# Kernel optimization log

Hardware: AMD Instinct MI355X
Metric: run time of the kernel (lower is better)

Reference implementation:

```python
import jax, jax.numpy as jnp
import numpy as np

B, N, C = 4, 2048, 768
H = 12
D = C // H  # head_dim = 64


def setup_inputs() -> dict:
    key = jax.random.key(0)
    k1, k2, k3, k4, k5 = jax.random.split(key, 5)
    s = 0.02
    return {
        "x": jax.random.normal(k1, (B, N, C), dtype=jnp.float32),
        "qkv_w": jax.random.normal(k2, (3 * C, C), dtype=jnp.float32) * s,
        "qkv_b": jax.random.normal(k3, (3 * C,), dtype=jnp.float32) * s,
        "proj_w": jax.random.normal(k4, (C, C), dtype=jnp.float32) * s,
        "proj_b": jax.random.normal(k5, (C,), dtype=jnp.float32) * s,
    }


def reference(x, qkv_w, qkv_b, proj_w, proj_b):
    b, n, c = x.shape
    # qkv projection (torch Linear: x @ W.T + b) -> [B,N,3,H,D] -> [3,B,H,N,D]
    qkv = (x @ qkv_w.T + qkv_b).reshape(b, n, 3, H, D).transpose(2, 0, 3, 1, 4)
    q, k, v = qkv[0], qkv[1], qkv[2]
    scale = D ** (-0.5)
    attn = jnp.einsum("bhqd,bhkd->bhqk", q, k) * scale
    attn = jax.nn.softmax(attn, axis=-1)
    # dropout is identity in eval mode
    out = jnp.einsum("bhqk,bhkd->bhqd", attn, v)  # [B,H,N,D]
    out = out.transpose(0, 2, 1, 3).reshape(b, n, c)
    return out @ proj_w.T + proj_b
```

## Files before the change

### kernel.cpp

```cpp
#include <hip/hip_runtime.h>
#include <hip/hip_bf16.h>
#include <stdint.h>

typedef __bf16 bf16_t;
typedef __bf16 bf16x8 __attribute__((ext_vector_type(8)));
typedef float f32x4 __attribute__((ext_vector_type(4)));
typedef unsigned int u32x4 __attribute__((ext_vector_type(4)));

#define NB 4
#define NH 12
#define ND 64
#define NN 2048
#define NC 768

__device__ __forceinline__ void async_copy16(const bf16_t* g, bf16_t* l) {
    __builtin_amdgcn_global_load_lds((__attribute__((address_space(1))) void*)(void*)g,
                                     (__attribute__((address_space(3))) void*)l, 16, 0, 0);
}

__device__ __forceinline__ unsigned pack_bf2(float a, float b) {
    union { bf16_t e[2]; unsigned u; } t;
    t.e[0] = (bf16_t)a;
    t.e[1] = (bf16_t)b;
    return t.u;
}

__global__ void cast_kernel(const float* __restrict__ src, bf16_t* __restrict__ dst, int n4) {
    int i = blockIdx.x * blockDim.x + threadIdx.x;
    if (i >= n4) return;
    float4 v = ((const float4*)src)[i];
    union { bf16_t e[4]; uint2 u; } t;
    t.e[0] = (bf16_t)v.x; t.e[1] = (bf16_t)v.y; t.e[2] = (bf16_t)v.z; t.e[3] = (bf16_t)v.w;
    ((uint2*)dst)[i] = t.u;
}

__device__ __forceinline__ int vperm(int s) {
    return (s & 32) | (((s >> 2) & 3) << 3) | (((s >> 4) & 1) << 2) | (s & 3);
}


template <bool ISV>
__launch_bounds__(256)
__global__ void qkv_gemm_kernel(const bf16_t* __restrict__ X, const bf16_t* __restrict__ W,
                                const float* __restrict__ bias,
                                bf16_t* __restrict__ Q, bf16_t* __restrict__ K, bf16_t* __restrict__ V,
                                int n0base)
{
    __shared__ __align__(16) bf16_t sA[128 * 64];
    __shared__ __align__(16) bf16_t sB[128 * 64];
    const int tid  = threadIdx.x;
    const int lane = tid & 63;
    const int w    = tid >> 6;
    const int wm   = w & 1, wn = w >> 1;
    const int m0   = blockIdx.x * 128;
    const int n0   = n0base + blockIdx.y * 128;
    const int lrow = lane & 15;
    const int quad = lane >> 4;
    const int arow = lane >> 3;
    const int gch  = (lane & 7) ^ arow;

    const int colbase = n0 + wn * 64;

    f32x4 zero = {0.f, 0.f, 0.f, 0.f};
    f32x4 acc[4][4];
#pragma unroll
    for (int i = 0; i < 4; ++i)
#pragma unroll
        for (int j = 0; j < 4; ++j) acc[i][j] = zero;

    for (int kt = 0; kt < NC; kt += 64) {
        __syncthreads();
        for (int c = w; c < 16; c += 4) {
            async_copy16(X + (size_t)(m0 + c * 8 + arow) * NC + kt + gch * 8, sA + c * 512);
            async_copy16(W + (size_t)(n0 + c * 8 + arow) * NC + kt + gch * 8, sB + c * 512);
        }
        __syncthreads();
#pragma unroll
        for (int hh = 0; hh < 2; ++hh) {
            bf16x8 xf[4], wf[4];
#pragma unroll
            for (int i = 0; i < 4; ++i) {
                int r = wm * 64 + i * 16 + lrow;
                xf[i] = *(const bf16x8*)(sA + r * 64 + (((hh * 4 + quad) ^ (r & 7)) * 8));
            }
#pragma unroll
            for (int j = 0; j < 4; ++j) {
                int r = wn * 64 + j * 16 + lrow;
                wf[j] = *(const bf16x8*)(sB + r * 64 + (((hh * 4 + quad) ^ (r & 7)) * 8));
            }
#pragma unroll
            for (int i = 0; i < 4; ++i)
#pragma unroll
                for (int j = 0; j < 4; ++j) {
                    if (ISV)
                        acc[i][j] = __builtin_amdgcn_mfma_f32_16x16x32_bf16(xf[i], wf[j], acc[i][j], 0, 0, 0);
                    else
                        acc[i][j] = __builtin_amdgcn_mfma_f32_16x16x32_bf16(wf[j], xf[i], acc[i][j], 0, 0, 0);
                }
        }
    }

    const float qscale = 0.125f * 1.44269504088896340736f;

    if (!ISV) {
        const int t3 = colbase / NC;
        const int h  = (colbase % NC) / ND;
        bf16_t* outb = t3 ? K : Q;
#pragma unroll
        for (int j = 0; j < 4; ++j) {
            const int dcol = j * 16 + quad * 4;
            const float4 bv4 = *(const float4*)(bias + colbase + dcol);
#pragma unroll
            for (int i = 0; i < 4; ++i) {
                const int tok = m0 + wm * 64 + i * 16 + lrow;
                const int bb = tok >> 11;
                const int nn = tok & 2047;
                union { bf16_t e[4]; uint2 u; } pk;
#pragma unroll
                for (int p = 0; p < 4; ++p) {
                    float val = acc[i][j][p] + (&bv4.x)[p];
                    if (t3 == 0) val *= qscale;
                    pk.e[p] = (bf16_t)val;
                }
                *(uint2*)(outb + ((size_t)(bb * NH + h) * NN + nn) * ND + dcol) = pk.u;
            }
        }
    } else {
        const int h = (colbase - 2 * NC) / ND;
#pragma unroll
        for (int j = 0; j < 4; ++j) {
            const int d  = j * 16 + lrow;
            const float bv = bias[colbase + d];
#pragma unroll
            for (int i = 0; i < 4; ++i) {
                const int tok0 = m0 + wm * 64 + i * 16 + quad * 4;
                const int bb = tok0 >> 11;
                const int nn = tok0 & 2047;
                union { bf16_t e[4]; uint2 u; } pk;
#pragma unroll
                for (int p = 0; p < 4; ++p) pk.e[p] = (bf16_t)(acc[i][j][p] + bv);
                const int pos = (nn & ~63) | vperm(nn & 63);
                *(uint2*)(V + ((size_t)(bb * NH + h) * ND + d) * NN + pos) = pk.u;
            }
        }
    }
}

__launch_bounds__(256, 4)
__global__ void attn_kernel(const bf16_t* __restrict__ Q, const bf16_t* __restrict__ K,
                            const bf16_t* __restrict__ Vt, bf16_t* __restrict__ O)
{
    __shared__ __align__(16) bf16_t sKV[4][64 * 64];
    bf16_t* sQ = sKV[0];
    const int tid  = threadIdx.x;
    const int lane = tid & 63;
    const int w    = tid >> 6;
    const int qt   = blockIdx.x;
    const int h    = blockIdx.y;
    const int b    = blockIdx.z;
    const int lrow = lane & 15;
    const int quad = lane >> 4;
    const int arow = lane >> 3;
    const int gch  = (lane & 7) ^ arow;
    const size_t head_off = (size_t)(b * NH + h) * NN * ND;
    const bf16_t* qh = Q  + head_off;
    const bf16_t* kh = K  + head_off;
    const bf16_t* vh = Vt + head_off;

#pragma unroll
    for (int c = 0; c < 4; ++c)
        async_copy16(qh + (size_t)(qt * 128 + (w * 4 + c) * 8 + arow) * ND + gch * 8,
                     sQ + (w * 4 + c) * 512);
    __syncthreads();

    bf16x8 qb[2][2];
#pragma unroll
    for (int qi = 0; qi < 2; ++qi)
#pragma unroll
        for (int hh = 0; hh < 2; ++hh) {
            int r = w * 32 + qi * 16 + lrow;
            qb[qi][hh] = *(const bf16x8*)(sQ + r * 64 + (((hh * 4 + quad) ^ (r & 7)) * 8));
        }

    int off[4][2];
#pragma unroll
    for (int blk = 0; blk < 4; ++blk) {
        int r = blk * 16 + lrow;
        off[blk][0] = r * 64 + ((quad ^ (r & 7)) * 8);
        off[blk][1] = r * 64 + (((4 + quad) ^ (r & 7)) * 8);
    }

    f32x4 zero = {0.f, 0.f, 0.f, 0.f};
    f32x4 o[2][4];
#pragma unroll
    for (int qi = 0; qi < 2; ++qi)
#pragma unroll
        for (int db = 0; db < 4; ++db) o[qi][db] = zero;
    float l_i[2] = {0.f, 0.f};

    const bf16_t* kp = kh + (size_t)(w * 16 + arow) * ND + gch * 8;
    const bf16_t* vp = vh + (size_t)(w * 16 + arow) * NN + gch * 8;

    for (int it = 0; it < NN / 128; ++it) {
        __syncthreads();
        async_copy16(kp,               sKV[0] + w * 1024);
        async_copy16(kp + 8 * ND,      sKV[0] + w * 1024 + 512);
        async_copy16(kp + 64 * ND,     sKV[1] + w * 1024);
        async_copy16(kp + 72 * ND,     sKV[1] + w * 1024 + 512);
        async_copy16(vp,               sKV[2] + w * 1024);
        async_copy16(vp + 8 * NN,      sKV[2] + w * 1024 + 512);
        async_copy16(vp + 64,          sKV[3] + w * 1024);
        async_copy16(vp + 8 * NN + 64, sKV[3] + w * 1024 + 512);
        __syncthreads();
        kp += 128 * ND;
        vp += 128;

#pragma unroll
        for (int half = 0; half < 2; ++half) {
            const bf16_t* sKh = sKV[half];
            const bf16_t* sVh = sKV[2 + half];

            f32x4 s[2][4];
#pragma unroll
            for (int blk = 0; blk < 4; ++blk) {
                bf16x8 a0 = *(const bf16x8*)(sKh + off[blk][0]);
                bf16x8 a1 = *(const bf16x8*)(sKh + off[blk][1]);
#pragma unroll
                for (int qi = 0; qi < 2; ++qi) {
                    f32x4 z = zero;
                    z = __builtin_amdgcn_mfma_f32_16x16x32_bf16(a0, qb[qi][0], z, 0, 0, 0);
                    z = __builtin_amdgcn_mfma_f32_16x16x32_bf16(a1, qb[qi][1], z, 0, 0, 0);
                    s[qi][blk] = z;
                }
            }

            bf16x8 pe[2][2];
#pragma unroll
            for (int qi = 0; qi < 2; ++qi) {
                u32x4 pu0 = {0, 0, 0, 0}, pu1 = {0, 0, 0, 0};
                float r0 = 0.f, r1 = 0.f;
#pragma unroll
                for (int blk = 0; blk < 4; ++blk) {
                    float e0 = __builtin_amdgcn_exp2f(s[qi][blk][0]);
                    float e1 = __builtin_amdgcn_exp2f(s[qi][blk][1]);
                    float e2 = __builtin_amdgcn_exp2f(s[qi][blk][2]);
                    float e3 = __builtin_amdgcn_exp2f(s[qi][blk][3]);
                    r0 += e0 + e1;
                    r1 += e2 + e3;
                    unsigned lo = pack_bf2(e0, e1), hi = pack_bf2(e2, e3);
                    if (blk == 0)      { pu0[0] = lo; pu0[1] = hi; }
                    else if (blk == 1) { pu0[2] = lo; pu0[3] = hi; }
                    else if (blk == 2) { pu1[0] = lo; pu1[1] = hi; }
                    else               { pu1[2] = lo; pu1[3] = hi; }
                }
                pe[qi][0] = __builtin_bit_cast(bf16x8, pu0);
                pe[qi][1] = __builtin_bit_cast(bf16x8, pu1);
                l_i[qi] += r0 + r1;
            }

#pragma unroll
            for (int db = 0; db < 4; ++db) {
                bf16x8 v0 = *(const bf16x8*)(sVh + off[db][0]);
                bf16x8 v1 = *(const bf16x8*)(sVh + off[db][1]);
#pragma unroll
                for (int qi = 0; qi < 2; ++qi) {
                    o[qi][db] = __builtin_amdgcn_mfma_f32_16x16x32_bf16(v0, pe[qi][0], o[qi][db], 0, 0, 0);
                    o[qi][db] = __builtin_amdgcn_mfma_f32_16x16x32_bf16(v1, pe[qi][1], o[qi][db], 0, 0, 0);
                }
            }
        }
    }

#pragma unroll
    for (int qi = 0; qi < 2; ++qi) {
        float l = l_i[qi];
        l += __shfl_xor(l, 16);
        l += __shfl_xor(l, 32);
        const float rl = 1.0f / l;
        const int n = qt * 128 + w * 32 + qi * 16 + lrow;
        const size_t rowoff = ((size_t)(b * NN + n)) * NC + h * ND;
#pragma unroll
        for (int db = 0; db < 4; ++db) {
            union { bf16_t e[4]; uint2 u; } pk;
#pragma unroll
            for (int p = 0; p < 4; ++p) pk.e[p] = (bf16_t)(o[qi][db][p] * rl);
            *(uint2*)(O + rowoff + db * 16 + quad * 4) = pk.u;
        }
    }
}

__launch_bounds__(256)
__global__ void proj_gemm_kernel(const bf16_t* __restrict__ A, const bf16_t* __restrict__ W,
                                 const float* __restrict__ bias, float* __restrict__ out)
{
    __shared__ __align__(16) bf16_t sA[128 * 64];
    __shared__ __align__(16) bf16_t sB[128 * 64];
    const int tid  = threadIdx.x;
    const int lane = tid & 63;
    const int w    = tid >> 6;
    const int wm   = w & 1, wn = w >> 1;
    const int m0   = blockIdx.x * 128;
    const int n0   = blockIdx.y * 128;
    const int lrow = lane & 15;
    const int quad = lane >> 4;
    const int arow = lane >> 3;
    const int gch  = (lane & 7) ^ arow;

    f32x4 zero = {0.f, 0.f, 0.f, 0.f};
    f32x4 acc[4][4];
#pragma unroll
    for (int i = 0; i < 4; ++i)
#pragma unroll
        for (int j = 0; j < 4; ++j) acc[i][j] = zero;

    for (int kt = 0; kt < NC; kt += 64) {
        __syncthreads();
        for (int c = w; c < 16; c += 4) {
            async_copy16(A + (size_t)(m0 + c * 8 + arow) * NC + kt + gch * 8, sA + c * 512);
            async_copy16(W + (size_t)(n0 + c * 8 + arow) * NC + kt + gch * 8, sB + c * 512);
        }
        __syncthreads();
#pragma unroll
        for (int hh = 0; hh < 2; ++hh) {
            bf16x8 xf[4], wf[4];
#pragma unroll
            for (int i = 0; i < 4; ++i) {
                int r = wm * 64 + i * 16 + lrow;
                xf[i] = *(const bf16x8*)(sA + r * 64 + (((hh * 4 + quad) ^ (r & 7)) * 8));
            }
#pragma unroll
            for (int j = 0; j < 4; ++j) {
                int r = wn * 64 + j * 16 + lrow;
                wf[j] = *(const bf16x8*)(sB + r * 64 + (((hh * 4 + quad) ^ (r & 7)) * 8));
            }
#pragma unroll
            for (int i = 0; i < 4; ++i)
#pragma unroll
                for (int j = 0; j < 4; ++j)
                    acc[i][j] = __builtin_amdgcn_mfma_f32_16x16x32_bf16(wf[j], xf[i], acc[i][j], 0, 0, 0);
        }
    }

#pragma unroll
    for (int j = 0; j < 4; ++j) {
        const int colg0 = n0 + wn * 64 + j * 16 + quad * 4;
        const float4 bv4 = *(const float4*)(bias + colg0);
#pragma unroll
        for (int i = 0; i < 4; ++i) {
            const int tok = m0 + wm * 64 + i * 16 + lrow;
            float4 val;
#pragma unroll
            for (int p = 0; p < 4; ++p) (&val.x)[p] = acc[i][j][p] + (&bv4.x)[p];
            *(float4*)(out + (size_t)tok * NC + colg0) = val;
        }
    }
}

extern "C" void kernel_launch(void* const* d_in, const int* in_sizes, int n_in,
                              void* d_out, int out_size, void* d_ws, size_t ws_size,
                              hipStream_t stream) {
    const float* x      = (const float*)d_in[0];
    const float* qkv_w  = (const float*)d_in[1];
    const float* qkv_b  = (const float*)d_in[2];
    const float* proj_w = (const float*)d_in[3];
    const float* proj_b = (const float*)d_in[4];
    float* out = (float*)d_out;

    char* ws = (char*)d_ws;
    bf16_t* xb    = (bf16_t*)ws; ws += (size_t)8192 * 768 * 2;
    bf16_t* wqkv  = (bf16_t*)ws; ws += (size_t)2304 * 768 * 2;
    bf16_t* wproj = (bf16_t*)ws; ws += (size_t)768 * 768 * 2;
    bf16_t* qb    = (bf16_t*)ws; ws += (size_t)NB * NH * NN * ND * 2;
    bf16_t* kb    = (bf16_t*)ws; ws += (size_t)NB * NH * NN * ND * 2;
    bf16_t* vb    = (bf16_t*)ws; ws += (size_t)NB * NH * NN * ND * 2;
    bf16_t* ab    = (bf16_t*)ws; ws += (size_t)8192 * 768 * 2;

    cast_kernel<<<(8192 * 768 / 4 + 255) / 256, 256, 0, stream>>>(x, xb, 8192 * 768 / 4);
    cast_kernel<<<(2304 * 768 / 4 + 255) / 256, 256, 0, stream>>>(qkv_w, wqkv, 2304 * 768 / 4);
    cast_kernel<<<(768 * 768 / 4 + 255) / 256, 256, 0, stream>>>(proj_w, wproj, 768 * 768 / 4);

    qkv_gemm_kernel<false><<<dim3(8192 / 128, 12), 256, 0, stream>>>(xb, wqkv, qkv_b, qb, kb, vb, 0);
    qkv_gemm_kernel<true><<<dim3(8192 / 128, 6), 256, 0, stream>>>(xb, wqkv, qkv_b, qb, kb, vb, 1536);
    attn_kernel<<<dim3(NN / 128, NH, NB), 256, 0, stream>>>(qb, kb, vb, ab);
    proj_gemm_kernel<<<dim3(8192 / 128, 768 / 128), 256, 0, stream>>>(ab, wproj, proj_b, out);
}
```

Before: 238.7 us.

## Double-buffer LDS tiles in GEMM and attention kernels, merge cast launches

The QKV and projection GEMMs change from single-buffered 64-wide K tiles with two barriers per step to double-buffered 32-wide K tiles. The next tile's async global-to-LDS copy is issued before the current tile's MFMAs, so each step needs only one barrier. The attention kernel also double-buffers its 64-key K/V tiles to overlap loads with compute, and adds a barrier after reading Q from the shared buffer. The three fp32-to-bf16 cast launches become one kernel, and both GEMMs get an occupancy hint of 4 blocks. The costs are more loop iterations, more barriers in attention, and possible register pressure under the new launch bounds.

```diff
diff --git a/kernel.cpp b/kernel.cpp
--- a/kernel.cpp
+++ b/kernel.cpp
@@ -25,13 +25,21 @@
     return t.u;
 }
 
-__global__ void cast_kernel(const float* __restrict__ src, bf16_t* __restrict__ dst, int n4) {
+__global__ void cast3_kernel(const float* __restrict__ s0, bf16_t* __restrict__ d0, int n0,
+                             const float* __restrict__ s1, bf16_t* __restrict__ d1, int n1,
+                             const float* __restrict__ s2, bf16_t* __restrict__ d2, int n2) {
     int i = blockIdx.x * blockDim.x + threadIdx.x;
-    if (i >= n4) return;
-    float4 v = ((const float4*)src)[i];
+    const float* s;
+    bf16_t* d;
+    int j;
+    if (i < n0)           { s = s0; d = d0; j = i; }
+    else if (i < n0 + n1) { s = s1; d = d1; j = i - n0; }
+    else if (i < n0 + n1 + n2) { s = s2; d = d2; j = i - n0 - n1; }
+    else return;
+    float4 v = ((const float4*)s)[j];
     union { bf16_t e[4]; uint2 u; } t;
     t.e[0] = (bf16_t)v.x; t.e[1] = (bf16_t)v.y; t.e[2] = (bf16_t)v.z; t.e[3] = (bf16_t)v.w;
-    ((uint2*)dst)[i] = t.u;
+    ((uint2*)d)[j] = t.u;
 }
 
 __device__ __forceinline__ int vperm(int s) {
@@ -40,14 +48,14 @@
 
 
 template <bool ISV>
-__launch_bounds__(256)
+__launch_bounds__(256, 4)
 __global__ void qkv_gemm_kernel(const bf16_t* __restrict__ X, const bf16_t* __restrict__ W,
                                 const float* __restrict__ bias,
                                 bf16_t* __restrict__ Q, bf16_t* __restrict__ K, bf16_t* __restrict__ V,
                                 int n0base)
 {
-    __shared__ __align__(16) bf16_t sA[128 * 64];
-    __shared__ __align__(16) bf16_t sB[128 * 64];
+    __shared__ __align__(16) bf16_t sA[2][128 * 32];
+    __shared__ __align__(16) bf16_t sB[2][128 * 32];
     const int tid  = threadIdx.x;
     const int lane = tid & 63;
     const int w    = tid >> 6;
@@ -56,8 +64,12 @@
     const int n0   = n0base + blockIdx.y * 128;
     const int lrow = lane & 15;
     const int quad = lane >> 4;
-    const int arow = lane >> 3;
-    const int gch  = (lane & 7) ^ arow;
+
+    const int srow = w * 16 + (lane >> 2);
+    const int gchk = ((lane & 3) ^ (srow & 3)) * 8;
+    const bf16_t* pA = X + (size_t)(m0 + srow) * NC + gchk;
+    const bf16_t* pB = W + (size_t)(n0 + srow) * NC + gchk;
+    const int ldst = w * 512 + lane * 8;
 
     const int colbase = n0 + wn * 64;
 
@@ -68,36 +80,47 @@
 #pragma unroll
         for (int j = 0; j < 4; ++j) acc[i][j] = zero;
 
-    for (int kt = 0; kt < NC; kt += 64) {
+    int offA[4], offB[4];
+#pragma unroll
+    for (int i = 0; i < 4; ++i) {
+        int rA = wm * 64 + i * 16 + lrow;
+        int rB = wn * 64 + i * 16 + lrow;
+        offA[i] = rA * 32 + ((quad ^ (rA & 3)) * 8);
+        offB[i] = rB * 32 + ((quad ^ (rB & 3)) * 8);
+    }
+
+    async_copy16(pA,           sA[0] + ldst);
+    async_copy16(pA + 64 * NC, sA[0] + ldst + 2048);
+    async_copy16(pB,           sB[0] + ldst);
+    async_copy16(pB + 64 * NC, sB[0] + ldst + 2048);
+    pA += 32; pB += 32;
+    __syncthreads();
+
+    int cur = 0;
+    for (int it = 0; it < NC / 32; ++it) {
+        if (it + 1 < NC / 32) {
+            async_copy16(pA,           sA[cur ^ 1] + ldst);
+            async_copy16(pA + 64 * NC, sA[cur ^ 1] + ldst + 2048);
+            async_copy16(pB,           sB[cur ^ 1] + ldst);
+            async_copy16(pB + 64 * NC, sB[cur ^ 1] + ldst + 2048);
+            pA += 32; pB += 32;
+        }
+        bf16x8 xf[4], wf[4];
+#pragma unroll
+        for (int i = 0; i < 4; ++i) xf[i] = *(const bf16x8*)(sA[cur] + offA[i]);
+#pragma unroll
+        for (int j = 0; j < 4; ++j) wf[j] = *(const bf16x8*)(sB[cur] + offB[j]);
+#pragma unroll
+        for (int i = 0; i < 4; ++i)
+#pragma unroll
+            for (int j = 0; j < 4; ++j) {
+                if (ISV)
+                    acc[i][j] = __builtin_amdgcn_mfma_f32_16x16x32_bf16(xf[i], wf[j], acc[i][j], 0, 0, 0);
+                else
+                    acc[i][j] = __builtin_amdgcn_mfma_f32_16x16x32_bf16(wf[j], xf[i], acc[i][j], 0, 0, 0);
+            }
         __syncthreads();
-        for (int c = w; c < 16; c += 4) {
-            async_copy16(X + (size_t)(m0 + c * 8 + arow) * NC + kt + gch * 8, sA + c * 512);
-            async_copy16(W + (size_t)(n0 + c * 8 + arow) * NC + kt + gch * 8, sB + c * 512);
-        }
-        __syncthreads();
-#pragma unroll
-        for (int hh = 0; hh < 2; ++hh) {
-            bf16x8 xf[4], wf[4];
-#pragma unroll
-            for (int i = 0; i < 4; ++i) {
-                int r = wm * 64 + i * 16 + lrow;
-                xf[i] = *(const bf16x8*)(sA + r * 64 + (((hh * 4 + quad) ^ (r & 7)) * 8));
-            }
-#pragma unroll
-            for (int j = 0; j < 4; ++j) {
-                int r = wn * 64 + j * 16 + lrow;
-                wf[j] = *(const bf16x8*)(sB + r * 64 + (((hh * 4 + quad) ^ (r & 7)) * 8));
-            }
-#pragma unroll
-            for (int i = 0; i < 4; ++i)
-#pragma unroll
-                for (int j = 0; j < 4; ++j) {
-                    if (ISV)
-                        acc[i][j] = __builtin_amdgcn_mfma_f32_16x16x32_bf16(xf[i], wf[j], acc[i][j], 0, 0, 0);
-                    else
-                        acc[i][j] = __builtin_amdgcn_mfma_f32_16x16x32_bf16(wf[j], xf[i], acc[i][j], 0, 0, 0);
-                }
-        }
+        cur ^= 1;
     }
 
     const float qscale = 0.125f * 1.44269504088896340736f;
@@ -150,8 +173,9 @@
 __global__ void attn_kernel(const bf16_t* __restrict__ Q, const bf16_t* __restrict__ K,
                             const bf16_t* __restrict__ Vt, bf16_t* __restrict__ O)
 {
-    __shared__ __align__(16) bf16_t sKV[4][64 * 64];
-    bf16_t* sQ = sKV[0];
+    __shared__ __align__(16) bf16_t sK[2][64 * 64];
+    __shared__ __align__(16) bf16_t sV[2][64 * 64];
+    bf16_t* sQ = sK[0];
     const int tid  = threadIdx.x;
     const int lane = tid & 63;
     const int w    = tid >> 6;
@@ -181,6 +205,7 @@
             int r = w * 32 + qi * 16 + lrow;
             qb[qi][hh] = *(const bf16x8*)(sQ + r * 64 + (((hh * 4 + quad) ^ (r & 7)) * 8));
         }
+    __syncthreads();
 
     int off[4][2];
 #pragma unroll
@@ -200,75 +225,79 @@
 
     const bf16_t* kp = kh + (size_t)(w * 16 + arow) * ND + gch * 8;
     const bf16_t* vp = vh + (size_t)(w * 16 + arow) * NN + gch * 8;
-
-    for (int it = 0; it < NN / 128; ++it) {
+    const int ldst = w * 1024 + (lane & 7) * 8 + 0;
+
+    async_copy16(kp,          sK[0] + w * 1024);
+    async_copy16(kp + 8 * ND, sK[0] + w * 1024 + 512);
+    async_copy16(vp,          sV[0] + w * 1024);
+    async_copy16(vp + 8 * NN, sV[0] + w * 1024 + 512);
+    kp += 64 * ND; vp += 64;
+    __syncthreads();
+
+    int cur = 0;
+    for (int it = 0; it < NN / 64; ++it) {
+        if (it + 1 < NN / 64) {
+            bf16_t* dK = sK[cur ^ 1] + w * 1024;
+            bf16_t* dV = sV[cur ^ 1] + w * 1024;
+            async_copy16(kp,          dK);
+            async_copy16(kp + 8 * ND, dK + 512);
+            async_copy16(vp,          dV);
+            async_copy16(vp + 8 * NN, dV + 512);
+            kp += 64 * ND; vp += 64;
+        }
+        const bf16_t* sKh = sK[cur];
+        const bf16_t* sVh = sV[cur];
+
+        f32x4 s[2][4];
+#pragma unroll
+        for (int blk = 0; blk < 4; ++blk) {
+            bf16x8 a0 = *(const bf16x8*)(sKh + off[blk][0]);
+            bf16x8 a1 = *(const bf16x8*)(sKh + off[blk][1]);
+#pragma unroll
+            for (int qi = 0; qi < 2; ++qi) {
+                f32x4 z = zero;
+                z = __builtin_amdgcn_mfma_f32_16x16x32_bf16(a0, qb[qi][0], z, 0, 0, 0);
+                z = __builtin_amdgcn_mfma_f32_16x16x32_bf16(a1, qb[qi][1], z, 0, 0, 0);
+                s[qi][blk] = z;
+            }
+        }
+
+        bf16x8 pe[2][2];
+#pragma unroll
+        for (int qi = 0; qi < 2; ++qi) {
+            u32x4 pu0 = {0, 0, 0, 0}, pu1 = {0, 0, 0, 0};
+            float r0 = 0.f, r1 = 0.f;
+#pragma unroll
+            for (int blk = 0; blk < 4; ++blk) {
+                float e0 = __builtin_amdgcn_exp2f(s[qi][blk][0]);
+                float e1 = __builtin_amdgcn_exp2f(s[qi][blk][1]);
+                float e2 = __builtin_amdgcn_exp2f(s[qi][blk][2]);
+                float e3 = __builtin_amdgcn_exp2f(s[qi][blk][3]);
+                r0 += e0 + e1;
+                r1 += e2 + e3;
+                unsigned lo = pack_bf2(e0, e1), hi = pack_bf2(e2, e3);
+                if (blk == 0)      { pu0[0] = lo; pu0[1] = hi; }
+                else if (blk == 1) { pu0[2] = lo; pu0[3] = hi; }
+                else if (blk == 2) { pu1[0] = lo; pu1[1] = hi; }
+                else               { pu1[2] = lo; pu1[3] = hi; }
+            }
+            pe[qi][0] = __builtin_bit_cast(bf16x8, pu0);
+            pe[qi][1] = __builtin_bit_cast(bf16x8, pu1);
+            l_i[qi] += r0 + r1;
+        }
+
+#pragma unroll
+        for (int db = 0; db < 4; ++db) {
+            bf16x8 v0 = *(const bf16x8*)(sVh + off[db][0]);
+            bf16x8 v1 = *(const bf16x8*)(sVh + off[db][1]);
+#pragma unroll
+            for (int qi = 0; qi < 2; ++qi) {
+                o[qi][db] = __builtin_amdgcn_mfma_f32_16x16x32_bf16(v0, pe[qi][0], o[qi][db], 0, 0, 0);
+                o[qi][db] = __builtin_amdgcn_mfma_f32_16x16x32_bf16(v1, pe[qi][1], o[qi][db], 0, 0, 0);
+            }
+        }
         __syncthreads();
-        async_copy16(kp,               sKV[0] + w * 1024);
-        async_copy16(kp + 8 * ND,      sKV[0] + w * 1024 + 512);
-        async_copy16(kp + 64 * ND,     sKV[1] + w * 1024);
-        async_copy16(kp + 72 * ND,     sKV[1] + w * 1024 + 512);
-        async_copy16(vp,               sKV[2] + w * 1024);
-        async_copy16(vp + 8 * NN,      sKV[2] + w * 1024 + 512);
-        async_copy16(vp + 64,          sKV[3] + w * 1024);
-        async_copy16(vp + 8 * NN + 64, sKV[3] + w * 1024 + 512);
-        __syncthreads();
-        kp += 128 * ND;
-        vp += 128;
-
-#pragma unroll
-        for (int half = 0; half < 2; ++half) {
-            const bf16_t* sKh = sKV[half];
-            const bf16_t* sVh = sKV[2 + half];
-
-            f32x4 s[2][4];
-#pragma unroll
-            for (int blk = 0; blk < 4; ++blk) {
-                bf16x8 a0 = *(const bf16x8*)(sKh + off[blk][0]);
-                bf16x8 a1 = *(const bf16x8*)(sKh + off[blk][1]);
-#pragma unroll
-                for (int qi = 0; qi < 2; ++qi) {
-                    f32x4 z = zero;
-                    z = __builtin_amdgcn_mfma_f32_16x16x32_bf16(a0, qb[qi][0], z, 0, 0, 0);
-                    z = __builtin_amdgcn_mfma_f32_16x16x32_bf16(a1, qb[qi][1], z, 0, 0, 0);
-                    s[qi][blk] = z;
-                }
-            }
-
-            bf16x8 pe[2][2];
-#pragma unroll
-            for (int qi = 0; qi < 2; ++qi) {
-                u32x4 pu0 = {0, 0, 0, 0}, pu1 = {0, 0, 0, 0};
-                float r0 = 0.f, r1 = 0.f;
-#pragma unroll
-                for (int blk = 0; blk < 4; ++blk) {
-                    float e0 = __builtin_amdgcn_exp2f(s[qi][blk][0]);
-                    float e1 = __builtin_amdgcn_exp2f(s[qi][blk][1]);
-                    float e2 = __builtin_amdgcn_exp2f(s[qi][blk][2]);
-                    float e3 = __builtin_amdgcn_exp2f(s[qi][blk][3]);
-                    r0 += e0 + e1;
-                    r1 += e2 + e3;
-                    unsigned lo = pack_bf2(e0, e1), hi = pack_bf2(e2, e3);
-                    if (blk == 0)      { pu0[0] = lo; pu0[1] = hi; }
-                    else if (blk == 1) { pu0[2] = lo; pu0[3] = hi; }
-                    else if (blk == 2) { pu1[0] = lo; pu1[1] = hi; }
-                    else               { pu1[2] = lo; pu1[3] = hi; }
-                }
-                pe[qi][0] = __builtin_bit_cast(bf16x8, pu0);
-                pe[qi][1] = __builtin_bit_cast(bf16x8, pu1);
-                l_i[qi] += r0 + r1;
-            }
-
-#pragma unroll
-            for (int db = 0; db < 4; ++db) {
-                bf16x8 v0 = *(const bf16x8*)(sVh + off[db][0]);
-                bf16x8 v1 = *(const bf16x8*)(sVh + off[db][1]);
-#pragma unroll
-                for (int qi = 0; qi < 2; ++qi) {
-                    o[qi][db] = __builtin_amdgcn_mfma_f32_16x16x32_bf16(v0, pe[qi][0], o[qi][db], 0, 0, 0);
-                    o[qi][db] = __builtin_amdgcn_mfma_f32_16x16x32_bf16(v1, pe[qi][1], o[qi][db], 0, 0, 0);
-                }
-            }
-        }
+        cur ^= 1;
     }
 
 #pragma unroll
@@ -289,12 +318,12 @@
     }
 }
 
-__launch_bounds__(256)
+__launch_bounds__(256, 4)
 __global__ void proj_gemm_kernel(const bf16_t* __restrict__ A, const bf16_t* __restrict__ W,
                                  const float* __restrict__ bias, float* __restrict__ out)
 {
-    __shared__ __align__(16) bf16_t sA[128 * 64];
-    __shared__ __align__(16) bf16_t sB[128 * 64];
+    __shared__ __align__(16) bf16_t sA[2][128 * 32];
+    __shared__ __align__(16) bf16_t sB[2][128 * 32];
     const int tid  = threadIdx.x;
     const int lane = tid & 63;
     const int w    = tid >> 6;
@@ -303,8 +332,12 @@
     const int n0   = blockIdx.y * 128;
     const int lrow = lane & 15;
     const int quad = lane >> 4;
-    const int arow = lane >> 3;
-    const int gch  = (lane & 7) ^ arow;
+
+    const int srow = w * 16 + (lane >> 2);
+    const int gchk = ((lane & 3) ^ (srow & 3)) * 8;
+    const bf16_t* pA = A + (size_t)(m0 + srow) * NC + gchk;
+    const bf16_t* pB = W + (size_t)(n0 + srow) * NC + gchk;
+    const int ldst = w * 512 + lane * 8;
 
     f32x4 zero = {0.f, 0.f, 0.f, 0.f};
     f32x4 acc[4][4];
@@ -313,32 +346,43 @@
 #pragma unroll
         for (int j = 0; j < 4; ++j) acc[i][j] = zero;
 
-    for (int kt = 0; kt < NC; kt += 64) {
+    int offA[4], offB[4];
+#pragma unroll
+    for (int i = 0; i < 4; ++i) {
+        int rA = wm * 64 + i * 16 + lrow;
+        int rB = wn * 64 + i * 16 + lrow;
+        offA[i] = rA * 32 + ((quad ^ (rA & 3)) * 8);
+        offB[i] = rB * 32 + ((quad ^ (rB & 3)) * 8);
+    }
+
+    async_copy16(pA,           sA[0] + ldst);
+    async_copy16(pA + 64 * NC, sA[0] + ldst + 2048);
+    async_copy16(pB,           sB[0] + ldst);
+    async_copy16(pB + 64 * NC, sB[0] + ldst + 2048);
+    pA += 32; pB += 32;
+    __syncthreads();
+
+    int cur = 0;
+    for (int it = 0; it < NC / 32; ++it) {
+        if (it + 1 < NC / 32) {
+            async_copy16(pA,           sA[cur ^ 1] + ldst);
+            async_copy16(pA + 64 * NC, sA[cur ^ 1] + ldst + 2048);
+            async_copy16(pB,           sB[cur ^ 1] + ldst);
+            async_copy16(pB + 64 * NC, sB[cur ^ 1] + ldst + 2048);
+            pA += 32; pB += 32;
+        }
+        bf16x8 xf[4], wf[4];
+#pragma unroll
+        for (int i = 0; i < 4; ++i) xf[i] = *(const bf16x8*)(sA[cur] + offA[i]);
+#pragma unroll
+        for (int j = 0; j < 4; ++j) wf[j] = *(const bf16x8*)(sB[cur] + offB[j]);
+#pragma unroll
+        for (int i = 0; i < 4; ++i)
+#pragma unroll
+            for (int j = 0; j < 4; ++j)
+                acc[i][j] = __builtin_amdgcn_mfma_f32_16x16x32_bf16(wf[j], xf[i], acc[i][j], 0, 0, 0);
         __syncthreads();
-        for (int c = w; c < 16; c += 4) {
-            async_copy16(A + (size_t)(m0 + c * 8 + arow) * NC + kt + gch * 8, sA + c * 512);
-            async_copy16(W + (size_t)(n0 + c * 8 + arow) * NC + kt + gch * 8, sB + c * 512);
-        }
-        __syncthreads();
-#pragma unroll
-        for (int hh = 0; hh < 2; ++hh) {
-            bf16x8 xf[4], wf[4];
-#pragma unroll
-            for (int i = 0; i < 4; ++i) {
-                int r = wm * 64 + i * 16 + lrow;
-                xf[i] = *(const bf16x8*)(sA + r * 64 + (((hh * 4 + quad) ^ (r & 7)) * 8));
-            }
-#pragma unroll
-            for (int j = 0; j < 4; ++j) {
-                int r = wn * 64 + j * 16 + lrow;
-                wf[j] = *(const bf16x8*)(sB + r * 64 + (((hh * 4 + quad) ^ (r & 7)) * 8));
-            }
-#pragma unroll
-            for (int i = 0; i < 4; ++i)
-#pragma unroll
-                for (int j = 0; j < 4; ++j)
-                    acc[i][j] = __builtin_amdgcn_mfma_f32_16x16x32_bf16(wf[j], xf[i], acc[i][j], 0, 0, 0);
-        }
+        cur ^= 1;
     }
 
 #pragma unroll
@@ -375,9 +419,8 @@
     bf16_t* vb    = (bf16_t*)ws; ws += (size_t)NB * NH * NN * ND * 2;
     bf16_t* ab    = (bf16_t*)ws; ws += (size_t)8192 * 768 * 2;
 
-    cast_kernel<<<(8192 * 768 / 4 + 255) / 256, 256, 0, stream>>>(x, xb, 8192 * 768 / 4);
-    cast_kernel<<<(2304 * 768 / 4 + 255) / 256, 256, 0, stream>>>(qkv_w, wqkv, 2304 * 768 / 4);
-    cast_kernel<<<(768 * 768 / 4 + 255) / 256, 256, 0, stream>>>(proj_w, wproj, 768 * 768 / 4);
+    const int c0 = 8192 * 768 / 4, c1 = 2304 * 768 / 4, c2 = 768 * 768 / 4;
+    cast3_kernel<<<(c0 + c1 + c2 + 255) / 256, 256, 0, stream>>>(x, xb, c0, qkv_w, wqkv, c1, proj_w, wproj, c2);
 
     qkv_gemm_kernel<false><<<dim3(8192 / 128, 12), 256, 0, stream>>>(xb, wqkv, qkv_b, qb, kb, vb, 0);
     qkv_gemm_kernel<true><<<dim3(8192 / 128, 6), 256, 0, stream>>>(xb, wqkv, qkv_b, qb, kb, vb, 1536);
```

Measured after the change: 220.7 us. 1.08x faster.
